# Kernel tuning notes

Hardware: AMD Instinct MI355X
Metric: run time of the kernel (lower is better)

The kernel has to match this reference:

```python
import jax, jax.numpy as jnp
import numpy as np

N_NODES = 100000
N_EDGES = 1600000


def setup_inputs() -> dict:
    key = jax.random.key(0)
    ks = jax.random.split(key, 5)
    x = jax.random.normal(ks[0], (N_NODES, 128), dtype=jnp.float32)
    edge_index = jax.random.randint(ks[1], (2, N_EDGES), 0, N_NODES, dtype=jnp.int64)
    edge_weight = jnp.ones((N_EDGES,), dtype=jnp.float32)
    W1 = jax.random.normal(ks[2], (128, 128), dtype=jnp.float32) * (1.0 / np.sqrt(128))
    b1 = jnp.zeros((128,), dtype=jnp.float32)
    W2 = jax.random.normal(ks[3], (128, 64), dtype=jnp.float32) * (1.0 / np.sqrt(128))
    b2 = jnp.zeros((64,), dtype=jnp.float32)
    return {"x": x, "edge_index": edge_index, "edge_weight": edge_weight,
            "W1": W1, "b1": b1, "W2": W2, "b2": b2}


def _gcn_conv(x, rows, cols, W, b, n_nodes):
    # GCNConv(normalize=True), unit edge weights (forward overwrites weights with ones)
    h = x @ W                                             # [N, out]
    ones_w = jnp.ones(rows.shape[0], dtype=x.dtype)
    deg = jax.ops.segment_sum(ones_w, cols, num_segments=n_nodes)   # in-degree at targets
    dinv = jnp.where(deg > 0, deg ** -0.5, 0.0)
    norm = dinv[rows] * dinv[cols]                        # [E+N]
    msg = h[rows] * norm[:, None]                         # gather + scale, memory-bound
    out = jax.ops.segment_sum(msg, cols, num_segments=n_nodes)
    return out + b


def reference(x, edge_index, edge_weight, W1, b1, W2, b2):
    n = x.shape[0]
    loop = jnp.arange(n, dtype=edge_index.dtype)
    rows = jnp.concatenate([edge_index[0], loop])         # self-loops (PyG default)
    cols = jnp.concatenate([edge_index[1], loop])
    h = jax.nn.relu(_gcn_conv(x, rows, cols, W1, b1, n))
    logits = _gcn_conv(h, rows, cols, W2, b2, n)
    return logits
```

## Files before the change

kernel.cpp:

```cpp
#include <hip/hip_runtime.h>
#include <hip/hip_fp16.h>


constexpr int NN = 100000;
constexpr int NE = 1600000;
constexpr int BSH = 7;
constexpr int NB = (NN + 127) >> BSH;
constexpr int NBLK = 256;
constexpr int EPB = NE / NBLK;
constexpr int TSTR = 784;

typedef _Float16 f16x8 __attribute__((ext_vector_type(8)));
typedef float f32x4 __attribute__((ext_vector_type(4)));

__global__ __launch_bounds__(256) void k_hist(const int* __restrict__ cols,
                                              int* __restrict__ table) {
  __shared__ int cnt[NB];
  for (int i = threadIdx.x; i < NB; i += 256) cnt[i] = 0;
  __syncthreads();
  int base = blockIdx.x * EPB;
  for (int i = threadIdx.x; i < EPB; i += 256)
    atomicAdd(&cnt[cols[base + i] >> BSH], 1);
  __syncthreads();
  for (int i = threadIdx.x; i < NB; i += 256)
    table[blockIdx.x * TSTR + i] = cnt[i];
}

__global__ __launch_bounds__(256) void k_scanT(const int* __restrict__ table,
                                               int* __restrict__ startOff,
                                               int* __restrict__ btot) {
  __shared__ int s[256];
  int b = blockIdx.x, t = threadIdx.x;
  int v = table[t * TSTR + b];
  s[t] = v;
  __syncthreads();
  for (int off = 1; off < 256; off <<= 1) {
    int tmp = (t >= off) ? s[t - off] : 0;
    __syncthreads();
    s[t] += tmp;
    __syncthreads();
  }
  startOff[t * TSTR + b] = s[t] - v;
  if (t == 255) btot[b] = s[t];
}

__global__ __launch_bounds__(256) void k_scanBkt(const int* __restrict__ btot,
                                                 int* __restrict__ bucketBase) {
  __shared__ int s[256];
  int t = threadIdx.x;
  int base = t * 4;
  int d0 = (base + 0 < NB) ? btot[base + 0] : 0;
  int d1 = (base + 1 < NB) ? btot[base + 1] : 0;
  int d2 = (base + 2 < NB) ? btot[base + 2] : 0;
  int d3 = (base + 3 < NB) ? btot[base + 3] : 0;
  int tsum = d0 + d1 + d2 + d3;
  s[t] = tsum;
  __syncthreads();
  for (int off = 1; off < 256; off <<= 1) {
    int tmp = (t >= off) ? s[t - off] : 0;
    __syncthreads();
    s[t] += tmp;
    __syncthreads();
  }
  int ex = s[t] - tsum;
  if (base + 0 < NB) bucketBase[base + 0] = ex;
  if (base + 1 < NB) bucketBase[base + 1] = ex + d0;
  if (base + 2 < NB) bucketBase[base + 2] = ex + d0 + d1;
  if (base + 3 < NB) bucketBase[base + 3] = ex + d0 + d1 + d2;
}

__global__ __launch_bounds__(256) void k_scat(const int* __restrict__ rows,
                                              const int* __restrict__ cols,
                                              const int* __restrict__ startOff,
                                              const int* __restrict__ bucketBase,
                                              unsigned* __restrict__ binned) {
  __shared__ int scnt[NB];
  int blk = blockIdx.x;
  for (int i = threadIdx.x; i < NB; i += 256)
    scnt[i] = bucketBase[i] + startOff[blk * TSTR + i];
  __syncthreads();
  int base = blk * EPB;
  for (int i = threadIdx.x; i < EPB; i += 256) {
    int c = cols[base + i];
    int r = rows[base + i];
    int pos = atomicAdd(&scnt[c >> BSH], 1);
    binned[pos] = ((unsigned)r << BSH) | (unsigned)(c & 127);
  }
}

__global__ __launch_bounds__(256) void k_fillb(const unsigned* __restrict__ binned,
                                               const int* __restrict__ bucketBase,
                                               const int* __restrict__ btot,
                                               int* __restrict__ rowptr,
                                               int* __restrict__ deg,
                                               float* __restrict__ dinv,
                                               int* __restrict__ srcIdx,
                                               const float4* __restrict__ x4,
                                               float2* __restrict__ y8) {
  __shared__ int cnt[128];
  __shared__ int sc[128];
  __shared__ int rp[128];
  __shared__ float sdv[128];
  int b = blockIdx.x;
  int nb0 = b << BSH;
  int nn = min(128, NN - nb0);
  int tid = threadIdx.x;
  if (tid < 128) cnt[tid] = 0;
  __syncthreads();
  int ebeg = bucketBase[b];
  int eend = ebeg + btot[b];
  for (int p = ebeg + tid; p < eend; p += 256)
    atomicAdd(&cnt[binned[p] & 127], 1);
  __syncthreads();
  int v = (tid < 128) ? cnt[tid] : 0;
  if (tid < 128) sc[tid] = v;
  __syncthreads();
  for (int off = 1; off < 128; off <<= 1) {
    int tmp = (tid < 128 && tid >= off) ? sc[tid - off] : 0;
    __syncthreads();
    if (tid < 128) sc[tid] += tmp;
    __syncthreads();
  }
  if (tid < 128) {
    int ex = sc[tid] - v;
    rp[tid] = ebeg + ex;
    float dv = rsqrtf((float)v + 1.0f);
    sdv[tid] = dv;
    if (tid < nn) {
      rowptr[nb0 + tid] = ebeg + ex;
      deg[nb0 + tid] = v;
      dinv[nb0 + tid] = dv;
    }
    cnt[tid] = 0;
  }
  __syncthreads();
  for (int p = ebeg + tid; p < eend; p += 256) {
    unsigned pk = binned[p];
    int cl = pk & 127;
    int local = atomicAdd(&cnt[cl], 1);
    srcIdx[rp[cl] + local] = (int)(pk >> BSH);
  }
  int tot = nn << 5;
  const float4* xb = x4 + ((size_t)nb0 << 5);
  float2* yb = y8 + ((size_t)nb0 << 5);
  for (int i = tid; i < tot; i += 256) {
    float s = sdv[i >> 5];
    float4 vv = xb[i];
    union { __half2 h[2]; float2 f; } u;
    u.h[0] = __floats2half2_rn(vv.x * s, vv.y * s);
    u.h[1] = __floats2half2_rn(vv.z * s, vv.w * s);
    yb[i] = u.f;
  }
}

__global__ __launch_bounds__(256) void k_wt(const float* __restrict__ W1,
                                            const float* __restrict__ W2,
                                            __half* __restrict__ Wt1,
                                            __half* __restrict__ Wt2) {
  int i = blockIdx.x * 256 + threadIdx.x;
  if (i < 16384) {
    int k = i >> 7, n = i & 127;
    Wt1[n * 128 + k] = __float2half(W1[i]);
  } else {
    int j = i - 16384;
    int k = j >> 6, n = j & 63;
    Wt2[n * 128 + k] = __float2half(W2[j]);
  }
}

__global__ __launch_bounds__(256, 6) void k_fused(
    const __half* __restrict__ y, const int* __restrict__ rowptr,
    const int* __restrict__ deg, const int* __restrict__ srcIdx,
    const float* __restrict__ dinv, const __half* __restrict__ Wt1,
    const float* __restrict__ b1, const __half* __restrict__ Wt2,
    __half* __restrict__ z) {
  __shared__ __align__(16) __half sA[4][16][136];
  const int w = threadIdx.x >> 6, l = threadIdx.x & 63;
  const int rowTop = blockIdx.x * 64 + w * 16;
  if (rowTop >= NN) return;
  const int quad = l >> 4, m = l & 15;
  const int sb = l & 48;

  for (int p = 0; p < 4; ++p) {
    int node = rowTop + p * 4 + quad;
    int d = deg[node];
    int ptr = rowptr[node];
    float acc[8];
#pragma unroll
    for (int i = 0; i < 8; i++) acc[i] = 0.0f;
    for (int base = 0; base < d; base += 16) {
      int cntv = min(16, d - base);
      int my = (m < cntv) ? srcIdx[ptr + base + m] : 0;
      int k = 0;
      for (; k + 2 <= cntv; k += 2) {
        int s0 = __shfl(my, sb + k);
        int s1 = __shfl(my, sb + k + 1);
        f16x8 v0 = *reinterpret_cast<const f16x8*>(y + (size_t)s0 * 128 + m * 8);
        f16x8 v1 = *reinterpret_cast<const f16x8*>(y + (size_t)s1 * 128 + m * 8);
#pragma unroll
        for (int i = 0; i < 8; i++) acc[i] += (float)v0[i];
#pragma unroll
        for (int i = 0; i < 8; i++) acc[i] += (float)v1[i];
      }
      if (k < cntv) {
        int s0 = __shfl(my, sb + k);
        f16x8 v0 = *reinterpret_cast<const f16x8*>(y + (size_t)s0 * 128 + m * 8);
#pragma unroll
        for (int i = 0; i < 8; i++) acc[i] += (float)v0[i];
      }
    }
    f16x8 sv = *reinterpret_cast<const f16x8*>(y + (size_t)node * 128 + m * 8);
    float scn = dinv[node];
    f16x8 o;
#pragma unroll
    for (int i = 0; i < 8; i++) o[i] = (_Float16)((acc[i] + (float)sv[i]) * scn);
    *reinterpret_cast<f16x8*>(&sA[w][p * 4 + quad][m * 8]) = o;
  }

  f16x8 afrag[4];
#pragma unroll
  for (int kk = 0; kk < 4; kk++)
    afrag[kk] = *reinterpret_cast<const f16x8*>(&sA[w][m][kk * 32 + quad * 8]);
  f32x4 acc1[8];
#pragma unroll
  for (int t = 0; t < 8; t++) {
    float bv = b1[t * 16 + m];
    acc1[t] = (f32x4){bv, bv, bv, bv};
  }
#pragma unroll
  for (int kk = 0; kk < 4; kk++) {
#pragma unroll
    for (int t = 0; t < 8; t++) {
      f16x8 b = *reinterpret_cast<const f16x8*>(
          Wt1 + (size_t)(t * 16 + m) * 128 + kk * 32 + quad * 8);
      acc1[t] = __builtin_amdgcn_mfma_f32_16x16x32_f16(afrag[kk], b, acc1[t], 0, 0, 0);
    }
  }
#pragma unroll
  for (int t = 0; t < 8; t++)
#pragma unroll
    for (int i = 0; i < 4; i++)
      sA[w][quad * 4 + i][t * 16 + m] = __float2half(fmaxf(acc1[t][i], 0.0f));

  f16x8 hfrag[4];
#pragma unroll
  for (int kk = 0; kk < 4; kk++)
    hfrag[kk] = *reinterpret_cast<const f16x8*>(&sA[w][m][kk * 32 + quad * 8]);
  f32x4 acc2[4];
#pragma unroll
  for (int t = 0; t < 4; t++) acc2[t] = (f32x4){0.f, 0.f, 0.f, 0.f};
#pragma unroll
  for (int kk = 0; kk < 4; kk++) {
#pragma unroll
    for (int t = 0; t < 4; t++) {
      f16x8 b = *reinterpret_cast<const f16x8*>(
          Wt2 + (size_t)(t * 16 + m) * 128 + kk * 32 + quad * 8);
      acc2[t] = __builtin_amdgcn_mfma_f32_16x16x32_f16(hfrag[kk], b, acc2[t], 0, 0, 0);
    }
  }
  float rs[4];
#pragma unroll
  for (int i = 0; i < 4; i++) rs[i] = dinv[rowTop + quad * 4 + i];
#pragma unroll
  for (int t = 0; t < 4; t++)
#pragma unroll
    for (int i = 0; i < 4; i++)
      sA[w][quad * 4 + i][t * 16 + m] = __float2half(acc2[t][i] * rs[i]);

#pragma unroll
  for (int rep = 0; rep < 2; rep++) {
    int idx = rep * 64 + l;
    int r = idx >> 3, cc = idx & 7;
    *reinterpret_cast<float4*>(z + (size_t)(rowTop + r) * 64 + cc * 8) =
        *reinterpret_cast<const float4*>(&sA[w][r][cc * 8]);
  }
}

__global__ __launch_bounds__(256) void k_gath2(const __half* __restrict__ z,
                                               const int* __restrict__ rowptr,
                                               const int* __restrict__ deg,
                                               const int* __restrict__ srcIdx,
                                               const float* __restrict__ dinv,
                                               const float* __restrict__ b2,
                                               float* __restrict__ out) {
  int node = blockIdx.x * 4 + (threadIdx.x >> 6);
  if (node >= NN) return;
  int lane = threadIdx.x & 63;
  int g = lane >> 3;
  int c = lane & 7;
  int d = deg[node];
  int p = rowptr[node];
  size_t coff = (size_t)c * 8;
  float acc[8];
#pragma unroll
  for (int i = 0; i < 8; i++) acc[i] = 0.0f;

  for (int base = 0; base < d; base += 64) {
    int cnt = min(64, d - base);
    int my = (lane < cnt) ? srcIdx[p + base + lane] : 0;
    int k = 0;
    for (; k + 16 <= cnt; k += 16) {
      int s0 = __shfl(my, k + g);
      int s1 = __shfl(my, k + 8 + g);
      f16x8 v0 = *reinterpret_cast<const f16x8*>(z + (size_t)s0 * 64 + coff);
      f16x8 v1 = *reinterpret_cast<const f16x8*>(z + (size_t)s1 * 64 + coff);
#pragma unroll
      for (int i = 0; i < 8; i++) acc[i] += (float)v0[i];
#pragma unroll
      for (int i = 0; i < 8; i++) acc[i] += (float)v1[i];
    }
    for (; k < cnt; k += 8) {
      int idx = k + g;
      bool valid = idx < cnt;
      int s0 = __shfl(my, valid ? idx : 0);
      f16x8 v0 = *reinterpret_cast<const f16x8*>(z + (size_t)s0 * 64 + coff);
      if (valid) {
#pragma unroll
        for (int i = 0; i < 8; i++) acc[i] += (float)v0[i];
      }
    }
  }
#pragma unroll
  for (int i = 0; i < 8; i++) acc[i] += __shfl_xor(acc[i], 8);
#pragma unroll
  for (int i = 0; i < 8; i++) acc[i] += __shfl_xor(acc[i], 16);
#pragma unroll
  for (int i = 0; i < 8; i++) acc[i] += __shfl_xor(acc[i], 32);
  if (g == 0) {
    f16x8 sv = *reinterpret_cast<const f16x8*>(z + (size_t)node * 64 + coff);
    float s = dinv[node];
    const float4* b4 = reinterpret_cast<const float4*>(b2);
    float4 bv0 = b4[2 * c], bv1 = b4[2 * c + 1];
    float4 o0, o1;
    o0.x = (acc[0] + (float)sv[0]) * s + bv0.x;
    o0.y = (acc[1] + (float)sv[1]) * s + bv0.y;
    o0.z = (acc[2] + (float)sv[2]) * s + bv0.z;
    o0.w = (acc[3] + (float)sv[3]) * s + bv0.w;
    o1.x = (acc[4] + (float)sv[4]) * s + bv1.x;
    o1.y = (acc[5] + (float)sv[5]) * s + bv1.y;
    o1.z = (acc[6] + (float)sv[6]) * s + bv1.z;
    o1.w = (acc[7] + (float)sv[7]) * s + bv1.w;
    float4* op = reinterpret_cast<float4*>(out + (size_t)node * 64 + coff);
    op[0] = o0;
    op[1] = o1;
  }
}

extern "C" void kernel_launch(void* const* d_in, const int* in_sizes, int n_in,
                              void* d_out, int out_size, void* d_ws, size_t ws_size,
                              hipStream_t stream) {
  const float* x  = (const float*)d_in[0];
  const int*   ei = (const int*)d_in[1];
  const int* rows = ei;
  const int* cols = ei + NE;
  const float* W1 = (const float*)d_in[3];
  const float* b1 = (const float*)d_in[4];
  const float* W2 = (const float*)d_in[5];
  const float* b2 = (const float*)d_in[6];
  float* out = (float*)d_out;

  char* base = (char*)d_ws;
  constexpr size_t MB = 1 << 20;
  int*      deg       = (int*)(base + 0 * MB);
  int*      rowptr    = (int*)(base + 1 * MB);
  float*    dinv      = (float*)(base + 2 * MB);
  int*      btot      = (int*)(base + 3 * MB);
  int*      bucketBase= (int*)(base + 3 * MB + 16 * 1024);
  __half*   Wt1       = (__half*)(base + 3 * MB + 64 * 1024);
  __half*   Wt2       = (__half*)(base + 3 * MB + 128 * 1024);
  int*      table     = (int*)(base + 4 * MB);
  int*      startOff  = (int*)(base + 5 * MB);
  unsigned* binned    = (unsigned*)(base + 6 * MB);
  int*      srcIdx    = (int*)(base + 13 * MB);
  __half*   y         = (__half*)(base + 20 * MB);
  __half*   z         = (__half*)(base + 46 * MB);

  k_wt<<<96, 256, 0, stream>>>(W1, W2, Wt1, Wt2);
  k_hist<<<NBLK, 256, 0, stream>>>(cols, table);
  k_scanT<<<NB, 256, 0, stream>>>(table, startOff, btot);
  k_scanBkt<<<1, 256, 0, stream>>>(btot, bucketBase);
  k_scat<<<NBLK, 256, 0, stream>>>(rows, cols, startOff, bucketBase, binned);
  k_fillb<<<NB, 256, 0, stream>>>(binned, bucketBase, btot, rowptr, deg, dinv,
                                  srcIdx, (const float4*)x, (float2*)y);
  k_fused<<<(NN + 63) / 64, 256, 0, stream>>>(y, rowptr, deg, srcIdx, dinv,
                                              Wt1, b1, Wt2, z);
  k_gath2<<<(NN + 3) / 4, 256, 0, stream>>>(z, rowptr, deg, srcIdx, dinv, b2, out);
}
```

Baseline: 318.1 us.

## Gather each node with a full wavefront and split fused GEMMs across block warps

The fused layer-1 kernel now gives each node's neighbour gather a whole 64-lane wavefront, with four quads handling different edges, instead of one 16-lane quad per node. The partial sums are then combined with cross-quad shuffles. Blocks shrink to 32 nodes, and the two small MFMA GEMMs are split across the four warps by row and column tiles through shared memory, with block-wide barriers in between. The aim is more memory-level parallelism per node and higher occupancy (launch bounds 6 to 8). The cost is extra shuffle reductions, idle lanes on low-degree nodes, and added __syncthreads.

```diff
diff --git a/kernel.cpp b/kernel.cpp
--- a/kernel.cpp
+++ b/kernel.cpp
@@ -168,111 +168,127 @@
   }
 }
 
-__global__ __launch_bounds__(256, 6) void k_fused(
+__global__ __launch_bounds__(256, 8) void k_fused(
     const __half* __restrict__ y, const int* __restrict__ rowptr,
     const int* __restrict__ deg, const int* __restrict__ srcIdx,
     const float* __restrict__ dinv, const __half* __restrict__ Wt1,
     const float* __restrict__ b1, const __half* __restrict__ Wt2,
     __half* __restrict__ z) {
-  __shared__ __align__(16) __half sA[4][16][136];
+  __shared__ __align__(16) __half sA[32][136];
+  __shared__ __align__(16) __half sB[32][136];
   const int w = threadIdx.x >> 6, l = threadIdx.x & 63;
-  const int rowTop = blockIdx.x * 64 + w * 16;
-  if (rowTop >= NN) return;
+  const int blk0 = blockIdx.x * 32;
   const int quad = l >> 4, m = l & 15;
-  const int sb = l & 48;
-
-  for (int p = 0; p < 4; ++p) {
-    int node = rowTop + p * 4 + quad;
-    int d = deg[node];
-    int ptr = rowptr[node];
+
+  for (int i = 0; i < 8; ++i) {
+    const int lr = w * 8 + i;
+    const int node = blk0 + lr;
+    const int d = deg[node];
+    const int ptr = rowptr[node];
     float acc[8];
 #pragma unroll
-    for (int i = 0; i < 8; i++) acc[i] = 0.0f;
-    for (int base = 0; base < d; base += 16) {
-      int cntv = min(16, d - base);
-      int my = (m < cntv) ? srcIdx[ptr + base + m] : 0;
+    for (int j = 0; j < 8; j++) acc[j] = 0.0f;
+    for (int base = 0; base < d; base += 64) {
+      int cnt = min(64, d - base);
+      int my = (l < cnt) ? srcIdx[ptr + base + l] : 0;
       int k = 0;
-      for (; k + 2 <= cntv; k += 2) {
-        int s0 = __shfl(my, sb + k);
-        int s1 = __shfl(my, sb + k + 1);
+      for (; k + 8 <= cnt; k += 8) {
+        int s0 = __shfl(my, k + quad);
+        int s1 = __shfl(my, k + 4 + quad);
         f16x8 v0 = *reinterpret_cast<const f16x8*>(y + (size_t)s0 * 128 + m * 8);
         f16x8 v1 = *reinterpret_cast<const f16x8*>(y + (size_t)s1 * 128 + m * 8);
 #pragma unroll
-        for (int i = 0; i < 8; i++) acc[i] += (float)v0[i];
-#pragma unroll
-        for (int i = 0; i < 8; i++) acc[i] += (float)v1[i];
+        for (int j = 0; j < 8; j++) acc[j] += (float)v0[j];
+#pragma unroll
+        for (int j = 0; j < 8; j++) acc[j] += (float)v1[j];
       }
-      if (k < cntv) {
-        int s0 = __shfl(my, sb + k);
+      for (; k < cnt; k += 4) {
+        int idx = k + quad;
+        bool valid = idx < cnt;
+        int s0 = __shfl(my, valid ? idx : 0);
         f16x8 v0 = *reinterpret_cast<const f16x8*>(y + (size_t)s0 * 128 + m * 8);
-#pragma unroll
-        for (int i = 0; i < 8; i++) acc[i] += (float)v0[i];
+        if (valid) {
+#pragma unroll
+          for (int j = 0; j < 8; j++) acc[j] += (float)v0[j];
+        }
       }
     }
-    f16x8 sv = *reinterpret_cast<const f16x8*>(y + (size_t)node * 128 + m * 8);
-    float scn = dinv[node];
-    f16x8 o;
-#pragma unroll
-    for (int i = 0; i < 8; i++) o[i] = (_Float16)((acc[i] + (float)sv[i]) * scn);
-    *reinterpret_cast<f16x8*>(&sA[w][p * 4 + quad][m * 8]) = o;
-  }
-
+#pragma unroll
+    for (int j = 0; j < 8; j++) acc[j] += __shfl_xor(acc[j], 16);
+#pragma unroll
+    for (int j = 0; j < 8; j++) acc[j] += __shfl_xor(acc[j], 32);
+    if (quad == 0) {
+      f16x8 sv = *reinterpret_cast<const f16x8*>(y + (size_t)node * 128 + m * 8);
+      float scn = dinv[node];
+      f16x8 o;
+#pragma unroll
+      for (int j = 0; j < 8; j++)
+        o[j] = (_Float16)((acc[j] + (float)sv[j]) * scn);
+      *reinterpret_cast<f16x8*>(&sA[lr][m * 8]) = o;
+    }
+  }
+  __syncthreads();
+
+  const int rt = (w >> 1) * 16;
+  const int ct = (w & 1) * 4;
   f16x8 afrag[4];
 #pragma unroll
   for (int kk = 0; kk < 4; kk++)
-    afrag[kk] = *reinterpret_cast<const f16x8*>(&sA[w][m][kk * 32 + quad * 8]);
-  f32x4 acc1[8];
-#pragma unroll
-  for (int t = 0; t < 8; t++) {
-    float bv = b1[t * 16 + m];
+    afrag[kk] = *reinterpret_cast<const f16x8*>(&sA[rt + m][kk * 32 + quad * 8]);
+  f32x4 acc1[4];
+#pragma unroll
+  for (int t = 0; t < 4; t++) {
+    float bv = b1[(ct + t) * 16 + m];
     acc1[t] = (f32x4){bv, bv, bv, bv};
   }
-#pragma unroll
-  for (int kk = 0; kk < 4; kk++) {
-#pragma unroll
-    for (int t = 0; t < 8; t++) {
-      f16x8 b = *reinterpret_cast<const f16x8*>(
-          Wt1 + (size_t)(t * 16 + m) * 128 + kk * 32 + quad * 8);
-      acc1[t] = __builtin_amdgcn_mfma_f32_16x16x32_f16(afrag[kk], b, acc1[t], 0, 0, 0);
-    }
-  }
-#pragma unroll
-  for (int t = 0; t < 8; t++)
-#pragma unroll
-    for (int i = 0; i < 4; i++)
-      sA[w][quad * 4 + i][t * 16 + m] = __float2half(fmaxf(acc1[t][i], 0.0f));
-
-  f16x8 hfrag[4];
-#pragma unroll
-  for (int kk = 0; kk < 4; kk++)
-    hfrag[kk] = *reinterpret_cast<const f16x8*>(&sA[w][m][kk * 32 + quad * 8]);
-  f32x4 acc2[4];
-#pragma unroll
-  for (int t = 0; t < 4; t++) acc2[t] = (f32x4){0.f, 0.f, 0.f, 0.f};
 #pragma unroll
   for (int kk = 0; kk < 4; kk++) {
 #pragma unroll
     for (int t = 0; t < 4; t++) {
       f16x8 b = *reinterpret_cast<const f16x8*>(
-          Wt2 + (size_t)(t * 16 + m) * 128 + kk * 32 + quad * 8);
+          Wt1 + (size_t)((ct + t) * 16 + m) * 128 + kk * 32 + quad * 8);
+      acc1[t] = __builtin_amdgcn_mfma_f32_16x16x32_f16(afrag[kk], b, acc1[t], 0, 0, 0);
+    }
+  }
+#pragma unroll
+  for (int t = 0; t < 4; t++)
+#pragma unroll
+    for (int i = 0; i < 4; i++)
+      sB[rt + quad * 4 + i][(ct + t) * 16 + m] =
+          __float2half(fmaxf(acc1[t][i], 0.0f));
+  __syncthreads();
+
+  const int c2 = (w & 1) * 2;
+  f16x8 hfrag[4];
+#pragma unroll
+  for (int kk = 0; kk < 4; kk++)
+    hfrag[kk] = *reinterpret_cast<const f16x8*>(&sB[rt + m][kk * 32 + quad * 8]);
+  f32x4 acc2[2];
+#pragma unroll
+  for (int t = 0; t < 2; t++) acc2[t] = (f32x4){0.f, 0.f, 0.f, 0.f};
+#pragma unroll
+  for (int kk = 0; kk < 4; kk++) {
+#pragma unroll
+    for (int t = 0; t < 2; t++) {
+      f16x8 b = *reinterpret_cast<const f16x8*>(
+          Wt2 + (size_t)((c2 + t) * 16 + m) * 128 + kk * 32 + quad * 8);
       acc2[t] = __builtin_amdgcn_mfma_f32_16x16x32_f16(hfrag[kk], b, acc2[t], 0, 0, 0);
     }
   }
   float rs[4];
 #pragma unroll
-  for (int i = 0; i < 4; i++) rs[i] = dinv[rowTop + quad * 4 + i];
-#pragma unroll
-  for (int t = 0; t < 4; t++)
+  for (int i = 0; i < 4; i++) rs[i] = dinv[blk0 + rt + quad * 4 + i];
+#pragma unroll
+  for (int t = 0; t < 2; t++)
 #pragma unroll
     for (int i = 0; i < 4; i++)
-      sA[w][quad * 4 + i][t * 16 + m] = __float2half(acc2[t][i] * rs[i]);
-
-#pragma unroll
-  for (int rep = 0; rep < 2; rep++) {
-    int idx = rep * 64 + l;
-    int r = idx >> 3, cc = idx & 7;
-    *reinterpret_cast<float4*>(z + (size_t)(rowTop + r) * 64 + cc * 8) =
-        *reinterpret_cast<const float4*>(&sA[w][r][cc * 8]);
+      sA[rt + quad * 4 + i][(c2 + t) * 16 + m] = __float2half(acc2[t][i] * rs[i]);
+  __syncthreads();
+
+  {
+    int r = threadIdx.x >> 3, cc = threadIdx.x & 7;
+    *reinterpret_cast<float4*>(z + (size_t)(blk0 + r) * 64 + cc * 8) =
+        *reinterpret_cast<const float4*>(&sA[r][cc * 8]);
   }
 }
 
@@ -382,7 +398,7 @@
   k_scat<<<NBLK, 256, 0, stream>>>(rows, cols, startOff, bucketBase, binned);
   k_fillb<<<NB, 256, 0, stream>>>(binned, bucketBase, btot, rowptr, deg, dinv,
                                   srcIdx, (const float4*)x, (float2*)y);
-  k_fused<<<(NN + 63) / 64, 256, 0, stream>>>(y, rowptr, deg, srcIdx, dinv,
-                                              Wt1, b1, Wt2, z);
+  k_fused<<<NN / 32, 256, 0, stream>>>(y, rowptr, deg, srcIdx, dinv,
+                                       Wt1, b1, Wt2, z);
   k_gath2<<<(NN + 3) / 4, 256, 0, stream>>>(z, rowptr, deg, srcIdx, dinv, b2, out);
 }
```

After: 295.9 us. 1.07x faster.
